# Optimization experiments

Hardware: AMD Instinct MI355X
Metric: run time of the kernel (lower is better)

Reference implementation:

```python
import jax, jax.numpy as jnp
import numpy as np

PLANE_AXES = jnp.array([[[0., 1., 0.], [1., 0., 0.], [0., 0., 1.]],
                        [[0., 0., 1.], [1., 0., 0.], [0., 1., 0.]],
                        [[0., 1., 0.], [0., 0., 1.], [1., 0., 0.]]], dtype=jnp.float32)


def setup_inputs() -> dict:
    key = jax.random.key(0)
    k1, k2 = jax.random.split(key)
    M, C, R = 1048576, 32, 512
    coords = jax.random.uniform(k1, (M, 3), jnp.float32, -1.0, 1.0)
    triplane = jax.random.normal(k2, (1, 3, C, R, R), jnp.float32) * 0.1
    return {"coords": coords, "triplane": triplane}


def _bilinear_sample(plane, x, y):
    # plane: [C, R, R]; x, y: [M] pixel coords (align_corners=True mapping applied).
    # Matches torch grid_sample(mode='bilinear', padding_mode='zeros', align_corners=True).
    R = plane.shape[-1]
    x0 = jnp.floor(x)
    y0 = jnp.floor(y)
    x0i = x0.astype(jnp.int32)
    y0i = y0.astype(jnp.int32)
    wx1 = x - x0
    wx0 = 1.0 - wx1
    wy1 = y - y0
    wy0 = 1.0 - wy1

    def tap(xi, yi, w):
        valid = ((xi >= 0) & (xi < R) & (yi >= 0) & (yi < R)).astype(plane.dtype)
        xc = jnp.clip(xi, 0, R - 1)
        yc = jnp.clip(yi, 0, R - 1)
        return plane[:, yc, xc] * (w * valid)  # [C, M]

    return (tap(x0i, y0i, wx0 * wy0) + tap(x0i + 1, y0i, wx1 * wy0)
            + tap(x0i, y0i + 1, wx0 * wy1) + tap(x0i + 1, y0i + 1, wx1 * wy1))


def reference(coords, triplane):
    # coords: [M, 3]; triplane: [1, 3, C, R, R]
    _, P, C, R, _ = triplane.shape
    planes = jnp.clip(triplane.reshape(P, C, R, R), -1.0, 1.0)
    inv = jnp.linalg.inv(PLANE_AXES)  # [3, 3, 3]
    # project_onto_planes: bmm(coords, inv_planes), keep first two coords (x, y)
    proj = jnp.einsum('mc,pcd->pmd', coords, inv)[..., :2]  # [3, M, 2]
    px = (proj[..., 0] + 1.0) * 0.5 * (R - 1)  # align_corners=True
    py = (proj[..., 1] + 1.0) * 0.5 * (R - 1)
    feat = jax.vmap(_bilinear_sample)(planes, px, py)  # [3, C, M]
    return feat.sum(0).T  # [M, C] — sum across the 3 planes
```

## Files before the change

### kernel.cpp

```cpp
#include <hip/hip_runtime.h>
#include <hip/hip_bf16.h>
#include <stdint.h>

#define RES 512
#define CH  32
#define NP  3
#define NTEX (NP * RES * RES)
#define NT2  (NTEX / 2)
#define TEX_BYTES ((size_t)NTEX * CH * sizeof(uint16_t))
#define BGRID 16
#define NBIN  (BGRID * BGRID * BGRID)
#define HBLK  16384

typedef float vfloat4 __attribute__((ext_vector_type(4)));
typedef float vfloat2 __attribute__((ext_vector_type(2)));

static __device__ __forceinline__ uint16_t f2bf(float f) {
    union { float f; uint32_t u; } v; v.f = f;
    uint32_t u = v.u;
    uint32_t r = (u + 0x7fffu + ((u >> 16) & 1u)) >> 16;
    return (uint16_t)r;
}

static __device__ __forceinline__ int binq(float c) {
    int v = (int)floorf((c + 1.f) * (BGRID * 0.5f));
    return min(BGRID - 1, max(0, v));
}
static __device__ __forceinline__ int bin_of(float cx, float cy, float cz) {
    return (binq(cz) * BGRID + binq(cy)) * BGRID + binq(cx);
}

static __device__ __forceinline__ int xcd_swz(int bid, int nwg) {
    int q = nwg >> 3, r = nwg & 7;
    int k = bid & 7, i = bid >> 3;
    int base = (k < r) ? k * (q + 1) : r * (q + 1) + (k - r) * q;
    return base + i;
}

__global__ __launch_bounds__(256) void k_transpose(const float* __restrict__ tri,
                                                   uint16_t* __restrict__ ws) {
    int t2 = blockIdx.x * 256 + threadIdx.x;
    if (t2 >= NT2) return;
    int xp = t2 & (RES / 2 - 1);
    int y  = (t2 >> 8) & (RES - 1);
    int p  = t2 >> 17;
    int x  = xp * 2;
    const float* src = tri + (size_t)p * CH * RES * RES + (size_t)y * RES + x;
    uint32_t pa[16], pb[16];
#pragma unroll
    for (int i = 0; i < 16; ++i) {
        vfloat2 f0 = __builtin_nontemporal_load((const vfloat2*)&src[(size_t)(2 * i + 0) * (RES * RES)]);
        vfloat2 f1 = __builtin_nontemporal_load((const vfloat2*)&src[(size_t)(2 * i + 1) * (RES * RES)]);
        float a0 = fminf(1.f, fmaxf(-1.f, f0.x));
        float a1 = fminf(1.f, fmaxf(-1.f, f1.x));
        float b0 = fminf(1.f, fmaxf(-1.f, f0.y));
        float b1 = fminf(1.f, fmaxf(-1.f, f1.y));
        pa[i] = (uint32_t)f2bf(a0) | ((uint32_t)f2bf(a1) << 16);
        pb[i] = (uint32_t)f2bf(b0) | ((uint32_t)f2bf(b1) << 16);
    }
    uint4* dst = (uint4*)(ws + (size_t)(2 * t2) * CH);
#pragma unroll
    for (int i = 0; i < 4; ++i)
        dst[i] = make_uint4(pa[4 * i], pa[4 * i + 1], pa[4 * i + 2], pa[4 * i + 3]);
#pragma unroll
    for (int i = 0; i < 4; ++i)
        dst[4 + i] = make_uint4(pb[4 * i], pb[4 * i + 1], pb[4 * i + 2], pb[4 * i + 3]);
}

__global__ __launch_bounds__(1024) void k_hist2(const float* __restrict__ coords,
                                                uint32_t* __restrict__ bh, int M) {
    __shared__ uint32_t hl[NBIN];
    for (int i = threadIdx.x; i < NBIN; i += 1024) hl[i] = 0;
    __syncthreads();
    int base = blockIdx.x * HBLK;
#pragma unroll
    for (int k = 0; k < HBLK / 1024; ++k) {
        int m = base + k * 1024 + threadIdx.x;
        if (m < M) {
            float cx = coords[3 * m + 0];
            float cy = coords[3 * m + 1];
            float cz = coords[3 * m + 2];
            atomicAdd(&hl[bin_of(cx, cy, cz)], 1u);
        }
    }
    __syncthreads();
    uint32_t* row = bh + (size_t)blockIdx.x * NBIN;
    for (int i = threadIdx.x; i < NBIN; i += 1024) row[i] = hl[i];
}

__global__ __launch_bounds__(256) void k_scan1(uint32_t* __restrict__ bh,
                                               uint32_t* __restrict__ bintotal, int nblk) {
    int j = blockIdx.x * 256 + threadIdx.x;
    if (j >= NBIN) return;
    uint32_t run = 0;
#pragma unroll 4
    for (int b = 0; b < nblk; ++b) {
        size_t idx = (size_t)b * NBIN + j;
        uint32_t c = bh[idx];
        bh[idx] = run;
        run += c;
    }
    bintotal[j] = run;
}

__global__ __launch_bounds__(256) void k_base(const uint32_t* __restrict__ hist,
                                              uint32_t* __restrict__ cursor) {
    __shared__ uint32_t part[256];
    int tid = threadIdx.x;
    int b0 = tid * (NBIN / 256);
    uint32_t loc[NBIN / 256];
    uint32_t s = 0;
#pragma unroll
    for (int k = 0; k < NBIN / 256; ++k) { loc[k] = hist[b0 + k]; s += loc[k]; }
    part[tid] = s;
    __syncthreads();
    for (int off = 1; off < 256; off <<= 1) {
        uint32_t v = (tid >= off) ? part[tid - off] : 0u;
        __syncthreads();
        part[tid] += v;
        __syncthreads();
    }
    uint32_t run = part[tid] - s;
#pragma unroll
    for (int k = 0; k < NBIN / 256; ++k) { cursor[b0 + k] = run; run += loc[k]; }
}

__global__ __launch_bounds__(1024) void k_scatter2(const float* __restrict__ coords,
                                                   const uint32_t* __restrict__ bh,
                                                   const uint32_t* __restrict__ binbase,
                                                   float* __restrict__ csort, int M) {
    __shared__ uint32_t cur[NBIN];
    const uint32_t* row = bh + (size_t)blockIdx.x * NBIN;
    for (int i = threadIdx.x; i < NBIN; i += 1024) cur[i] = binbase[i] + row[i];
    __syncthreads();
    int base = blockIdx.x * HBLK;
#pragma unroll
    for (int k = 0; k < HBLK / 1024; ++k) {
        int m = base + k * 1024 + threadIdx.x;
        if (m < M) {
            float cx = coords[3 * m + 0];
            float cy = coords[3 * m + 1];
            float cz = coords[3 * m + 2];
            uint32_t pos = atomicAdd(&cur[bin_of(cx, cy, cz)], 1u);
            vfloat4 v = {cx, cy, cz, __uint_as_float((uint32_t)m)};
            __builtin_nontemporal_store(v, (vfloat4*)(csort + (size_t)pos * 4));
        }
    }
}

__global__ __launch_bounds__(256) void k_zero(uint32_t* __restrict__ hist) {
    int i = blockIdx.x * 256 + threadIdx.x;
    if (i < NBIN) hist[i] = 0;
}

__global__ __launch_bounds__(256) void k_hist(const float* __restrict__ coords,
                                              uint32_t* __restrict__ hist, int M) {
    __shared__ uint32_t hl[NBIN];
    for (int i = threadIdx.x; i < NBIN; i += 256) hl[i] = 0;
    __syncthreads();
    int base = blockIdx.x * 1024 + threadIdx.x;
#pragma unroll
    for (int k = 0; k < 4; ++k) {
        int m = base + k * 256;
        if (m < M) {
            float cx = coords[3 * m + 0];
            float cy = coords[3 * m + 1];
            float cz = coords[3 * m + 2];
            atomicAdd(&hl[bin_of(cx, cy, cz)], 1u);
        }
    }
    __syncthreads();
    for (int i = threadIdx.x; i < NBIN; i += 256) {
        uint32_t v = hl[i];
        if (v) atomicAdd(&hist[i], v);
    }
}

__global__ __launch_bounds__(256) void k_scatter(const float* __restrict__ coords,
                                                 uint32_t* __restrict__ cursor,
                                                 float4* __restrict__ csort, int M) {
    int m = blockIdx.x * 256 + threadIdx.x;
    if (m >= M) return;
    float cx = coords[3 * m + 0];
    float cy = coords[3 * m + 1];
    float cz = coords[3 * m + 2];
    uint32_t pos = atomicAdd(&cursor[bin_of(cx, cy, cz)], 1u);
    csort[pos] = make_float4(cx, cy, cz, __uint_as_float((uint32_t)m));
}

__global__ __launch_bounds__(256) void k_gather_sorted(const float* __restrict__ csort,
                                                       const uint16_t* __restrict__ tex,
                                                       float* __restrict__ out, int M) {
    int tid = threadIdx.x;
    int sub = tid & 3;
    int data = xcd_swz(blockIdx.x, gridDim.x);
    int i = data * 64 + (tid >> 2);
    if (i >= M) return;
    vfloat4 c4 = __builtin_nontemporal_load((const vfloat4*)(csort + (size_t)i * 4));
    float cx = c4.x, cy = c4.y, cz = c4.z;
    uint32_t mo = __float_as_uint(c4.w);

    float acc[8];
#pragma unroll
    for (int c = 0; c < 8; ++c) acc[c] = 0.f;

    float us[3] = {cy, cz, cy};
    float vs[3] = {cx, cx, cz};

#pragma unroll
    for (int p = 0; p < 3; ++p) {
        float px = (us[p] + 1.f) * (0.5f * (RES - 1));
        float py = (vs[p] + 1.f) * (0.5f * (RES - 1));
        float x0f = floorf(px), y0f = floorf(py);
        int x0 = (int)x0f, y0 = (int)y0f;
        float wx1 = px - x0f, wx0 = 1.f - wx1;
        float wy1 = py - y0f, wy0 = 1.f - wy1;
        int   xs[2]  = {x0, x0 + 1};
        int   ys[2]  = {y0, y0 + 1};
        float wxv[2] = {wx0, wx1};
        float wyv[2] = {wy0, wy1};
#pragma unroll
        for (int j = 0; j < 2; ++j) {
#pragma unroll
            for (int i2 = 0; i2 < 2; ++i2) {
                int xi = xs[i2], yi = ys[j];
                bool valid = (xi >= 0) & (xi < RES) & (yi >= 0) & (yi < RES);
                int xc = min(max(xi, 0), RES - 1);
                int yc = min(max(yi, 0), RES - 1);
                float w = valid ? (wxv[i2] * wyv[j]) : 0.f;
                const uint4* tp = (const uint4*)(tex + (((size_t)p * RES + yc) * RES + xc) * CH
                                                 + (size_t)sub * 8);
                uint4 d = *tp;
                uint32_t vv[4] = {d.x, d.y, d.z, d.w};
#pragma unroll
                for (int e = 0; e < 4; ++e) {
                    union { uint32_t u; float f; } lo, hi;
                    lo.u = vv[e] << 16;
                    hi.u = vv[e] & 0xffff0000u;
                    acc[2 * e + 0] += w * lo.f;
                    acc[2 * e + 1] += w * hi.f;
                }
            }
        }
    }

    vfloat4* dst = (vfloat4*)(out + (size_t)mo * CH + (size_t)sub * 8);
    vfloat4 v0 = {acc[0], acc[1], acc[2], acc[3]};
    vfloat4 v1 = {acc[4], acc[5], acc[6], acc[7]};
    __builtin_nontemporal_store(v0, dst);
    __builtin_nontemporal_store(v1, dst + 1);
}

__global__ __launch_bounds__(256) void k_gather(const float* __restrict__ coords,
                                                const uint16_t* __restrict__ ws,
                                                float* __restrict__ out, int M) {
    int tid = threadIdx.x;
    int sub = tid & 3;
    int m = blockIdx.x * 64 + (tid >> 2);
    if (m >= M) return;
    float cx = coords[3 * m + 0];
    float cy = coords[3 * m + 1];
    float cz = coords[3 * m + 2];
    float acc[8];
#pragma unroll
    for (int c = 0; c < 8; ++c) acc[c] = 0.f;
    float us[3] = {cy, cz, cy};
    float vs[3] = {cx, cx, cz};
#pragma unroll
    for (int p = 0; p < 3; ++p) {
        float px = (us[p] + 1.f) * (0.5f * (RES - 1));
        float py = (vs[p] + 1.f) * (0.5f * (RES - 1));
        float x0f = floorf(px), y0f = floorf(py);
        int x0 = (int)x0f, y0 = (int)y0f;
        float wx1 = px - x0f, wx0 = 1.f - wx1;
        float wy1 = py - y0f, wy0 = 1.f - wy1;
        int   xs[2]  = {x0, x0 + 1};
        int   ys[2]  = {y0, y0 + 1};
        float wxv[2] = {wx0, wx1};
        float wyv[2] = {wy0, wy1};
#pragma unroll
        for (int j = 0; j < 2; ++j) {
#pragma unroll
            for (int i = 0; i < 2; ++i) {
                int xi = xs[i], yi = ys[j];
                bool valid = (xi >= 0) & (xi < RES) & (yi >= 0) & (yi < RES);
                int xc = min(max(xi, 0), RES - 1);
                int yc = min(max(yi, 0), RES - 1);
                float w = valid ? (wxv[i] * wyv[j]) : 0.f;
                const uint4* tp = (const uint4*)(ws + (((size_t)p * RES + yc) * RES + xc) * CH
                                                 + (size_t)sub * 8);
                uint4 d = *tp;
                uint32_t vv[4] = {d.x, d.y, d.z, d.w};
#pragma unroll
                for (int e = 0; e < 4; ++e) {
                    union { uint32_t u; float f; } lo, hi;
                    lo.u = vv[e] << 16;
                    hi.u = vv[e] & 0xffff0000u;
                    acc[2 * e + 0] += w * lo.f;
                    acc[2 * e + 1] += w * hi.f;
                }
            }
        }
    }
    vfloat4* dst = (vfloat4*)(out + (size_t)m * CH + (size_t)sub * 8);
    vfloat4 v0 = {acc[0], acc[1], acc[2], acc[3]};
    vfloat4 v1 = {acc[4], acc[5], acc[6], acc[7]};
    __builtin_nontemporal_store(v0, dst);
    __builtin_nontemporal_store(v1, dst + 1);
}

__global__ __launch_bounds__(256) void k_gather_direct(const float* __restrict__ coords,
                                                       const float* __restrict__ tri,
                                                       float* __restrict__ out, int M) {
    int m = blockIdx.x * 256 + threadIdx.x;
    if (m >= M) return;
    float cx = coords[3 * m + 0];
    float cy = coords[3 * m + 1];
    float cz = coords[3 * m + 2];
    float acc[CH];
#pragma unroll
    for (int c = 0; c < CH; ++c) acc[c] = 0.f;
    float us[3] = {cy, cz, cy};
    float vs[3] = {cx, cx, cz};
    for (int p = 0; p < 3; ++p) {
        float px = (us[p] + 1.f) * (0.5f * (RES - 1));
        float py = (vs[p] + 1.f) * (0.5f * (RES - 1));
        float x0f = floorf(px), y0f = floorf(py);
        int x0 = (int)x0f, y0 = (int)y0f;
        float wx1 = px - x0f, wx0 = 1.f - wx1;
        float wy1 = py - y0f, wy0 = 1.f - wy1;
        int   xs[2]  = {x0, x0 + 1};
        int   ys[2]  = {y0, y0 + 1};
        float wxv[2] = {wx0, wx1};
        float wyv[2] = {wy0, wy1};
        for (int j = 0; j < 2; ++j)
            for (int i = 0; i < 2; ++i) {
                int xi = xs[i], yi = ys[j];
                bool valid = (xi >= 0) & (xi < RES) & (yi >= 0) & (yi < RES);
                int xc = min(max(xi, 0), RES - 1);
                int yc = min(max(yi, 0), RES - 1);
                float w = valid ? (wxv[i] * wyv[j]) : 0.f;
                const float* base = tri + ((size_t)p * CH) * RES * RES + (size_t)yc * RES + xc;
#pragma unroll
                for (int c = 0; c < CH; ++c) {
                    float v = base[(size_t)c * RES * RES];
                    v = fminf(1.f, fmaxf(-1.f, v));
                    acc[c] += w * v;
                }
            }
    }
    float4* dst = (float4*)(out + (size_t)m * CH);
#pragma unroll
    for (int i = 0; i < 8; ++i)
        dst[i] = make_float4(acc[4 * i], acc[4 * i + 1], acc[4 * i + 2], acc[4 * i + 3]);
}

extern "C" void kernel_launch(void* const* d_in, const int* in_sizes, int n_in,
                              void* d_out, int out_size, void* d_ws, size_t ws_size,
                              hipStream_t stream) {
    const float* coords = (const float*)d_in[0];
    const float* tri    = (const float*)d_in[1];
    float* out          = (float*)d_out;
    int M = in_sizes[0] / 3;
    int nblk = (M + HBLK - 1) / HBLK;
    int ngather = (M + 63) / 64;

    size_t off_csort = TEX_BYTES;
    size_t off_bh    = off_csort + (size_t)M * 16;
    size_t off_bt    = off_bh + (size_t)nblk * NBIN * 4;
    size_t off_bb    = off_bt + (size_t)NBIN * 4;
    size_t need_top  = off_bb + (size_t)NBIN * 4;

    size_t off_hist   = off_csort + (size_t)M * 16;
    size_t off_cursor = off_hist + (size_t)NBIN * 4;
    size_t need_mid   = off_cursor + (size_t)NBIN * 4;

    if (ws_size >= need_top) {
        uint16_t* tex    = (uint16_t*)d_ws;
        float*    csort  = (float*)((char*)d_ws + off_csort);
        uint32_t* bh     = (uint32_t*)((char*)d_ws + off_bh);
        uint32_t* bt     = (uint32_t*)((char*)d_ws + off_bt);
        uint32_t* bb     = (uint32_t*)((char*)d_ws + off_bb);
        k_transpose<<<(NT2 + 255) / 256, 256, 0, stream>>>(tri, tex);
        k_hist2<<<nblk, 1024, 0, stream>>>(coords, bh, M);
        k_scan1<<<(NBIN + 255) / 256, 256, 0, stream>>>(bh, bt, nblk);
        k_base<<<1, 256, 0, stream>>>(bt, bb);
        k_scatter2<<<nblk, 1024, 0, stream>>>(coords, bh, bb, csort, M);
        k_gather_sorted<<<ngather, 256, 0, stream>>>(csort, tex, out, M);
    } else if (ws_size >= need_mid) {
        uint16_t* tex    = (uint16_t*)d_ws;
        float*    csort  = (float*)((char*)d_ws + off_csort);
        uint32_t* hist   = (uint32_t*)((char*)d_ws + off_hist);
        uint32_t* cursor = (uint32_t*)((char*)d_ws + off_cursor);
        k_transpose<<<(NT2 + 255) / 256, 256, 0, stream>>>(tri, tex);
        k_zero<<<(NBIN + 255) / 256, 256, 0, stream>>>(hist);
        k_hist<<<(M + 1023) / 1024, 256, 0, stream>>>(coords, hist, M);
        k_base<<<1, 256, 0, stream>>>(hist, cursor);
        k_scatter<<<(M + 255) / 256, 256, 0, stream>>>(coords, cursor, (float4*)csort, M);
        k_gather_sorted<<<ngather, 256, 0, stream>>>(csort, tex, out, M);
    } else if (ws_size >= TEX_BYTES) {
        uint16_t* ws = (uint16_t*)d_ws;
        k_transpose<<<(NT2 + 255) / 256, 256, 0, stream>>>(tri, ws);
        k_gather<<<ngather, 256, 0, stream>>>(coords, ws, out, M);
    } else {
        k_gather_direct<<<(M + 255) / 256, 256, 0, stream>>>(coords, tri, out, M);
    }
}
```

Before: 358.4 us.

## Fuse transpose with histogram, fold base scan into scatter, Morton-order bins

Merges the texture transpose and the per-block histogram into one launch, with the first blocks doing the transpose and the rest building histograms. The global exclusive scan over bin totals is recomputed redundantly inside each scatter block, which removes the separate single-block k_base launch. Bin indices switch from row-major to Morton order, so consecutive sorted points stay closer in 3D and texture locality in the gather should improve. In exchange each scatter block does extra scan work, and the fused kernel runs the transpose with 1024-thread blocks.

```diff
diff --git a/kernel.cpp b/kernel.cpp
--- a/kernel.cpp
+++ b/kernel.cpp
@@ -11,6 +11,7 @@
 #define BGRID 16
 #define NBIN  (BGRID * BGRID * BGRID)
 #define HBLK  16384
+#define TGRID (NT2 / 1024)
 
 typedef float vfloat4 __attribute__((ext_vector_type(4)));
 typedef float vfloat2 __attribute__((ext_vector_type(2)));
@@ -26,8 +27,12 @@
     int v = (int)floorf((c + 1.f) * (BGRID * 0.5f));
     return min(BGRID - 1, max(0, v));
 }
+static __device__ __forceinline__ uint32_t spread3(uint32_t v) {
+    return (v & 1u) | ((v & 2u) << 2) | ((v & 4u) << 4) | ((v & 8u) << 6);
+}
 static __device__ __forceinline__ int bin_of(float cx, float cy, float cz) {
-    return (binq(cz) * BGRID + binq(cy)) * BGRID + binq(cx);
+    return (int)(spread3((uint32_t)binq(cx)) | (spread3((uint32_t)binq(cy)) << 1)
+                 | (spread3((uint32_t)binq(cz)) << 2));
 }
 
 static __device__ __forceinline__ int xcd_swz(int bid, int nwg) {
@@ -37,10 +42,8 @@
     return base + i;
 }
 
-__global__ __launch_bounds__(256) void k_transpose(const float* __restrict__ tri,
-                                                   uint16_t* __restrict__ ws) {
-    int t2 = blockIdx.x * 256 + threadIdx.x;
-    if (t2 >= NT2) return;
+static __device__ __forceinline__ void transpose_body(const float* __restrict__ tri,
+                                                      uint16_t* __restrict__ ws, int t2) {
     int xp = t2 & (RES / 2 - 1);
     int y  = (t2 >> 8) & (RES - 1);
     int p  = t2 >> 17;
@@ -67,12 +70,20 @@
         dst[4 + i] = make_uint4(pb[4 * i], pb[4 * i + 1], pb[4 * i + 2], pb[4 * i + 3]);
 }
 
-__global__ __launch_bounds__(1024) void k_hist2(const float* __restrict__ coords,
-                                                uint32_t* __restrict__ bh, int M) {
+__global__ __launch_bounds__(1024) void k_prep(const float* __restrict__ tri,
+                                               uint16_t* __restrict__ ws,
+                                               const float* __restrict__ coords,
+                                               uint32_t* __restrict__ bh, int M) {
     __shared__ uint32_t hl[NBIN];
+    if ((int)blockIdx.x < TGRID) {
+        int t2 = blockIdx.x * 1024 + threadIdx.x;
+        if (t2 < NT2) transpose_body(tri, ws, t2);
+        return;
+    }
+    int hb = blockIdx.x - TGRID;
     for (int i = threadIdx.x; i < NBIN; i += 1024) hl[i] = 0;
     __syncthreads();
-    int base = blockIdx.x * HBLK;
+    int base = hb * HBLK;
 #pragma unroll
     for (int k = 0; k < HBLK / 1024; ++k) {
         int m = base + k * 1024 + threadIdx.x;
@@ -84,7 +95,7 @@
         }
     }
     __syncthreads();
-    uint32_t* row = bh + (size_t)blockIdx.x * NBIN;
+    uint32_t* row = bh + (size_t)hb * NBIN;
     for (int i = threadIdx.x; i < NBIN; i += 1024) row[i] = hl[i];
 }
 
@@ -103,35 +114,30 @@
     bintotal[j] = run;
 }
 
-__global__ __launch_bounds__(256) void k_base(const uint32_t* __restrict__ hist,
-                                              uint32_t* __restrict__ cursor) {
-    __shared__ uint32_t part[256];
+__global__ __launch_bounds__(1024) void k_scatter2(const float* __restrict__ coords,
+                                                   const uint32_t* __restrict__ bh,
+                                                   const uint32_t* __restrict__ bintotal,
+                                                   float* __restrict__ csort, int M) {
+    __shared__ uint32_t cur[NBIN];
+    __shared__ uint32_t part[1024];
     int tid = threadIdx.x;
-    int b0 = tid * (NBIN / 256);
-    uint32_t loc[NBIN / 256];
+    int b0 = tid * 4;
+    uint32_t loc[4];
     uint32_t s = 0;
 #pragma unroll
-    for (int k = 0; k < NBIN / 256; ++k) { loc[k] = hist[b0 + k]; s += loc[k]; }
+    for (int k = 0; k < 4; ++k) { loc[k] = bintotal[b0 + k]; s += loc[k]; }
     part[tid] = s;
     __syncthreads();
-    for (int off = 1; off < 256; off <<= 1) {
+    for (int off = 1; off < 1024; off <<= 1) {
         uint32_t v = (tid >= off) ? part[tid - off] : 0u;
         __syncthreads();
         part[tid] += v;
         __syncthreads();
     }
     uint32_t run = part[tid] - s;
-#pragma unroll
-    for (int k = 0; k < NBIN / 256; ++k) { cursor[b0 + k] = run; run += loc[k]; }
-}
-
-__global__ __launch_bounds__(1024) void k_scatter2(const float* __restrict__ coords,
-                                                   const uint32_t* __restrict__ bh,
-                                                   const uint32_t* __restrict__ binbase,
-                                                   float* __restrict__ csort, int M) {
-    __shared__ uint32_t cur[NBIN];
     const uint32_t* row = bh + (size_t)blockIdx.x * NBIN;
-    for (int i = threadIdx.x; i < NBIN; i += 1024) cur[i] = binbase[i] + row[i];
+#pragma unroll
+    for (int k = 0; k < 4; ++k) { cur[b0 + k] = run + row[b0 + k]; run += loc[k]; }
     __syncthreads();
     int base = blockIdx.x * HBLK;
 #pragma unroll
@@ -146,46 +152,6 @@
             __builtin_nontemporal_store(v, (vfloat4*)(csort + (size_t)pos * 4));
         }
     }
-}
-
-__global__ __launch_bounds__(256) void k_zero(uint32_t* __restrict__ hist) {
-    int i = blockIdx.x * 256 + threadIdx.x;
-    if (i < NBIN) hist[i] = 0;
-}
-
-__global__ __launch_bounds__(256) void k_hist(const float* __restrict__ coords,
-                                              uint32_t* __restrict__ hist, int M) {
-    __shared__ uint32_t hl[NBIN];
-    for (int i = threadIdx.x; i < NBIN; i += 256) hl[i] = 0;
-    __syncthreads();
-    int base = blockIdx.x * 1024 + threadIdx.x;
-#pragma unroll
-    for (int k = 0; k < 4; ++k) {
-        int m = base + k * 256;
-        if (m < M) {
-            float cx = coords[3 * m + 0];
-            float cy = coords[3 * m + 1];
-            float cz = coords[3 * m + 2];
-            atomicAdd(&hl[bin_of(cx, cy, cz)], 1u);
-        }
-    }
-    __syncthreads();
-    for (int i = threadIdx.x; i < NBIN; i += 256) {
-        uint32_t v = hl[i];
-        if (v) atomicAdd(&hist[i], v);
-    }
-}
-
-__global__ __launch_bounds__(256) void k_scatter(const float* __restrict__ coords,
-                                                 uint32_t* __restrict__ cursor,
-                                                 float4* __restrict__ csort, int M) {
-    int m = blockIdx.x * 256 + threadIdx.x;
-    if (m >= M) return;
-    float cx = coords[3 * m + 0];
-    float cy = coords[3 * m + 1];
-    float cz = coords[3 * m + 2];
-    uint32_t pos = atomicAdd(&cursor[bin_of(cx, cy, cz)], 1u);
-    csort[pos] = make_float4(cx, cy, cz, __uint_as_float((uint32_t)m));
 }
 
 __global__ __launch_bounds__(256) void k_gather_sorted(const float* __restrict__ csort,
@@ -249,6 +215,74 @@
     vfloat4 v1 = {acc[4], acc[5], acc[6], acc[7]};
     __builtin_nontemporal_store(v0, dst);
     __builtin_nontemporal_store(v1, dst + 1);
+}
+
+__global__ __launch_bounds__(256) void k_transpose(const float* __restrict__ tri,
+                                                   uint16_t* __restrict__ ws) {
+    int t2 = blockIdx.x * 256 + threadIdx.x;
+    if (t2 < NT2) transpose_body(tri, ws, t2);
+}
+
+__global__ __launch_bounds__(256) void k_zero(uint32_t* __restrict__ hist) {
+    int i = blockIdx.x * 256 + threadIdx.x;
+    if (i < NBIN) hist[i] = 0;
+}
+
+__global__ __launch_bounds__(256) void k_hist(const float* __restrict__ coords,
+                                              uint32_t* __restrict__ hist, int M) {
+    __shared__ uint32_t hl[NBIN];
+    for (int i = threadIdx.x; i < NBIN; i += 256) hl[i] = 0;
+    __syncthreads();
+    int base = blockIdx.x * 1024 + threadIdx.x;
+#pragma unroll
+    for (int k = 0; k < 4; ++k) {
+        int m = base + k * 256;
+        if (m < M) {
+            float cx = coords[3 * m + 0];
+            float cy = coords[3 * m + 1];
+            float cz = coords[3 * m + 2];
+            atomicAdd(&hl[bin_of(cx, cy, cz)], 1u);
+        }
+    }
+    __syncthreads();
+    for (int i = threadIdx.x; i < NBIN; i += 256) {
+        uint32_t v = hl[i];
+        if (v) atomicAdd(&hist[i], v);
+    }
+}
+
+__global__ __launch_bounds__(256) void k_base(const uint32_t* __restrict__ hist,
+                                              uint32_t* __restrict__ cursor) {
+    __shared__ uint32_t part[256];
+    int tid = threadIdx.x;
+    int b0 = tid * (NBIN / 256);
+    uint32_t loc[NBIN / 256];
+    uint32_t s = 0;
+#pragma unroll
+    for (int k = 0; k < NBIN / 256; ++k) { loc[k] = hist[b0 + k]; s += loc[k]; }
+    part[tid] = s;
+    __syncthreads();
+    for (int off = 1; off < 256; off <<= 1) {
+        uint32_t v = (tid >= off) ? part[tid - off] : 0u;
+        __syncthreads();
+        part[tid] += v;
+        __syncthreads();
+    }
+    uint32_t run = part[tid] - s;
+#pragma unroll
+    for (int k = 0; k < NBIN / 256; ++k) { cursor[b0 + k] = run; run += loc[k]; }
+}
+
+__global__ __launch_bounds__(256) void k_scatter(const float* __restrict__ coords,
+                                                 uint32_t* __restrict__ cursor,
+                                                 float4* __restrict__ csort, int M) {
+    int m = blockIdx.x * 256 + threadIdx.x;
+    if (m >= M) return;
+    float cx = coords[3 * m + 0];
+    float cy = coords[3 * m + 1];
+    float cz = coords[3 * m + 2];
+    uint32_t pos = atomicAdd(&cursor[bin_of(cx, cy, cz)], 1u);
+    csort[pos] = make_float4(cx, cy, cz, __uint_as_float((uint32_t)m));
 }
 
 __global__ __launch_bounds__(256) void k_gather(const float* __restrict__ coords,
@@ -368,8 +402,7 @@
     size_t off_csort = TEX_BYTES;
     size_t off_bh    = off_csort + (size_t)M * 16;
     size_t off_bt    = off_bh + (size_t)nblk * NBIN * 4;
-    size_t off_bb    = off_bt + (size_t)NBIN * 4;
-    size_t need_top  = off_bb + (size_t)NBIN * 4;
+    size_t need_top  = off_bt + (size_t)NBIN * 4;
 
     size_t off_hist   = off_csort + (size_t)M * 16;
     size_t off_cursor = off_hist + (size_t)NBIN * 4;
@@ -380,12 +413,9 @@
         float*    csort  = (float*)((char*)d_ws + off_csort);
         uint32_t* bh     = (uint32_t*)((char*)d_ws + off_bh);
         uint32_t* bt     = (uint32_t*)((char*)d_ws + off_bt);
-        uint32_t* bb     = (uint32_t*)((char*)d_ws + off_bb);
-        k_transpose<<<(NT2 + 255) / 256, 256, 0, stream>>>(tri, tex);
-        k_hist2<<<nblk, 1024, 0, stream>>>(coords, bh, M);
+        k_prep<<<TGRID + nblk, 1024, 0, stream>>>(tri, tex, coords, bh, M);
         k_scan1<<<(NBIN + 255) / 256, 256, 0, stream>>>(bh, bt, nblk);
-        k_base<<<1, 256, 0, stream>>>(bt, bb);
-        k_scatter2<<<nblk, 1024, 0, stream>>>(coords, bh, bb, csort, M);
+        k_scatter2<<<nblk, 1024, 0, stream>>>(coords, bh, bt, csort, M);
         k_gather_sorted<<<ngather, 256, 0, stream>>>(csort, tex, out, M);
     } else if (ws_size >= need_mid) {
         uint16_t* tex    = (uint16_t*)d_ws;
```

Measured after the change: 361.1 us. About the same (+0.8%).
